# Optimization experiments

Hardware: AMD Instinct MI355X
Metric: run time of the kernel (lower is better)

The kernel has to match this reference:

```python
import jax, jax.numpy as jnp
import numpy as np

B, L, P, TPP, D, G = 4, 2, 100, 64, 768, 10  # batch, layers, passages, tokens/passage, hidden, n_tables
T = P * TPP


def setup_inputs() -> dict:
    key = jax.random.key(0)
    ks = jax.random.split(key, 12)
    s = 0.02  # weight init scale
    return {
        "answer_states": jax.random.normal(ks[0], (B, L, 1, D), jnp.float32),
        "query_passage_states": jax.random.normal(ks[1], (B, L, T, D), jnp.float32),
        "passage_masks": (jax.random.uniform(ks[2], (B, P, TPP)) < 0.9).astype(jnp.float32),
        "table_ids": jax.random.randint(ks[3], (B, P), 0, G, dtype=jnp.int32),
        "fusion_scores": jax.random.normal(ks[4], (B, P), jnp.float32),
        # learned params: passage_fnt (3D->D), table_fnt (3D->D), feat_l1 (2D->D), feat_l2 (D->1)
        "W_p": jax.random.normal(ks[5], (3 * D, D), jnp.float32) * s,
        "b_p": jnp.zeros((D,), jnp.float32),
        "W_t": jax.random.normal(ks[6], (3 * D, D), jnp.float32) * s,
        "b_t": jnp.zeros((D,), jnp.float32),
        "W1": jax.random.normal(ks[7], (2 * D, D), jnp.float32) * s,
        "b1": jnp.zeros((D,), jnp.float32),
        "W2": jax.random.normal(ks[8], (D, 1), jnp.float32) * s,
        "b2": jnp.zeros((1,), jnp.float32),
    }


def reference(answer_states, query_passage_states, passage_masks, table_ids,
              fusion_scores, W_p, b_p, W_t, b_t, W1, b1, W2, b2):
    # Use only the last layer, as in forward (states[:, -1:, :, :]).
    a = answer_states[:, -1:, :, :]                 # [B,1,1,D]
    q = query_passage_states[:, -1:, :, :]          # [B,1,T,D]
    a = jnp.broadcast_to(a, q.shape)
    x = jnp.concatenate([a, q, a * q], axis=-1)     # [B,1,T,3D]

    ps = (x @ W_p + b_p).reshape(B, 1, P, TPP, D)   # passage states
    ts = (x @ W_t + b_t).reshape(B, 1, P, TPP, D)   # per-passage table states

    # Group-by table_id max-pool over the passage axis, then broadcast back.
    def aggr_one(ts_i, tid):                        # ts_i: [1,P,TPP,D], tid: [P]
        data = jnp.moveaxis(ts_i, 1, 0)             # [P,1,TPP,D]
        seg_max = jax.ops.segment_max(data, tid, num_segments=G)  # [G,1,TPP,D]
        return jnp.moveaxis(seg_max[tid], 0, 1)     # [1,P,TPP,D]

    aggr = jax.vmap(aggr_one)(ts, table_ids)        # [B,1,P,TPP,D]

    feat = jnp.concatenate([ps, aggr], axis=-1)     # [B,1,P,TPP,2D]
    # feature_fnt: Linear -> ReLU -> (dropout = identity in eval) -> Linear
    h = jax.nn.relu(feat @ W1 + b1)                 # [B,1,P,TPP,D]
    scores = (h @ W2 + b2)[..., 0]                  # [B,1,P,TPP]

    masked = scores * passage_masks[:, None, :, :]  # broadcast mask over layers
    # sum over layers and tokens -> per-passage adapt scores
    out = masked.sum(axis=(1, 3))                   # [B,P]
    return out
```

## Files before the change

kernel.cpp:

```cpp
#include <hip/hip_runtime.h>
#include <hip/hip_bf16.h>

#define B_ 4
#define L_ 2
#define P_ 100
#define TPP_ 64
#define D_ 768
#define G_ 10
#define T_ (P_ * TPP_)
#define NC_ (2 * D_)

typedef __attribute__((ext_vector_type(8))) short bf16x8;
typedef __attribute__((ext_vector_type(4))) float f32x4;

__device__ __forceinline__ unsigned short f2bf(float f) {
    __hip_bfloat16 h = __float2bfloat16(f);
    return *reinterpret_cast<unsigned short*>(&h);
}
__device__ __forceinline__ float bfu2f(unsigned short u) {
    return __uint_as_float(((unsigned int)u) << 16);
}

__device__ __forceinline__ void gload_lds16(const void* g, void* l) {
    __builtin_amdgcn_global_load_lds(
        (const __attribute__((address_space(1))) void*)g,
        (__attribute__((address_space(3))) void*)l, 16, 0, 0);
}

#define SBAR()   __builtin_amdgcn_s_barrier()
#define SCHEDB() __builtin_amdgcn_sched_barrier(0)
#define VMCNT8() asm volatile("s_waitcnt vmcnt(8)" ::: "memory")
#define VMCNT0() asm volatile("s_waitcnt vmcnt(0)" ::: "memory")

__device__ __forceinline__ void stage64(
    const __hip_bfloat16* __restrict__ Ag, const __hip_bfloat16* __restrict__ Bg,
    int k0, __hip_bfloat16 (*As)[64], __hip_bfloat16 (*Bs)[64],
    int w, int row_l, int soff)
{
#pragma unroll
    for (int j = 0; j < 4; ++j) {
        int r = w * 32 + j * 8 + row_l;
        gload_lds16(Ag + (size_t)r * D_ + k0 + soff, &As[w * 32 + j * 8][0]);
        gload_lds16(Bg + (size_t)r * D_ + k0 + soff, &Bs[w * 32 + j * 8][0]);
    }
}

__device__ __forceinline__ void mfma_step64(
    __hip_bfloat16 (*As)[64], __hip_bfloat16 (*Bs)[64],
    int rr, int h, int wm, int wn, f32x4 acc[4][4])
{
#pragma unroll
    for (int ks = 0; ks < 2; ++ks) {
        const int rsl = (((ks << 2) + h) ^ (rr & 7)) << 3;
        bf16x8 af[4], bfr[4];
#pragma unroll
        for (int mi = 0; mi < 4; ++mi)
            af[mi] = *reinterpret_cast<const bf16x8*>(
                &As[wm * 64 + mi * 16 + rr][rsl]);
#pragma unroll
        for (int ni = 0; ni < 4; ++ni)
            bfr[ni] = *reinterpret_cast<const bf16x8*>(
                &Bs[wn * 64 + ni * 16 + rr][rsl]);
#pragma unroll
        for (int mi = 0; mi < 4; ++mi)
#pragma unroll
            for (int ni = 0; ni < 4; ++ni)
                acc[mi][ni] = __builtin_amdgcn_mfma_f32_16x16x32_bf16(
                    af[mi], bfr[ni], acc[mi][ni], 0, 0, 0);
    }
}

#define MFMA_STEP_P(As, Bs)                                                   \
    __builtin_amdgcn_s_setprio(1);                                            \
    mfma_step64(As, Bs, rr, h, wm, wn, acc);                                  \
    __builtin_amdgcn_s_setprio(0);

#define MFMA_LOOP_PIPE(Ag, Bg)                                                \
    {                                                                         \
        const int rr = lane & 15, h = lane >> 4;                              \
        const int row_l = lane >> 3;                                          \
        const int soff = ((lane & 7) ^ row_l) << 3;                           \
        stage64((Ag), (Bg), 0, As0, Bs0, w, row_l, soff);                     \
        stage64((Ag), (Bg), 64, As1, Bs1, w, row_l, soff);                    \
        SCHEDB();                                                             \
        for (int t = 0; t < 10; t += 2) {                                     \
            VMCNT8(); SBAR(); SCHEDB();                                       \
            MFMA_STEP_P(As0, Bs0);                                            \
            SCHEDB(); SBAR(); SCHEDB();                                       \
            stage64((Ag), (Bg), (t + 2) * 64, As0, Bs0, w, row_l, soff);      \
            SCHEDB();                                                         \
            VMCNT8(); SBAR(); SCHEDB();                                       \
            MFMA_STEP_P(As1, Bs1);                                            \
            SCHEDB(); SBAR(); SCHEDB();                                       \
            stage64((Ag), (Bg), (t + 3) * 64, As1, Bs1, w, row_l, soff);      \
            SCHEDB();                                                         \
        }                                                                     \
        VMCNT8(); SBAR(); SCHEDB();                                           \
        MFMA_STEP_P(As0, Bs0);                                   \
        SCHEDB();                                                             \
        VMCNT0(); SBAR(); SCHEDB();                                           \
        MFMA_STEP_P(As1, Bs1);                                   \
        __syncthreads();                                                      \
    }

#define DECL_LDS_DB()                                                         \
    __shared__ __align__(16) __hip_bfloat16 As0[128][64];                     \
    __shared__ __align__(16) __hip_bfloat16 Bs0[128][64];                     \
    __shared__ __align__(16) __hip_bfloat16 As1[128][64];                     \
    __shared__ __align__(16) __hip_bfloat16 Bs1[128][64];

#define DECL_ACC()                                                            \
    f32x4 acc[4][4];                                                          \
    _Pragma("unroll") for (int i = 0; i < 4; ++i)                             \
        _Pragma("unroll") for (int j = 0; j < 4; ++j)                         \
            _Pragma("unroll") for (int e = 0; e < 4; ++e) acc[i][j][e] = 0.0f;

__global__ __launch_bounds__(256) void prep_all(
    const float* __restrict__ answer, const float* __restrict__ W_p,
    const float* __restrict__ b_p, const float* __restrict__ W_t,
    const float* __restrict__ b_t, const float* __restrict__ W1,
    const float* __restrict__ qps, const int* __restrict__ tids,
    const float* __restrict__ mask, const float* __restrict__ b2,
    __hip_bfloat16* __restrict__ Wpe_nat, __hip_bfloat16* __restrict__ Wbig,
    float* __restrict__ c_p, float* __restrict__ c_t,
    __hip_bfloat16* __restrict__ qb, __hip_bfloat16* __restrict__ W1at,
    __hip_bfloat16* __restrict__ W1bt, int* __restrict__ glist,
    int* __restrict__ goff, float* __restrict__ out)
{
    __shared__ float lds[64][65];
    __shared__ float a_s[64];
    __shared__ float red2[2][4][64];
    __shared__ int g_cnt[B_][G_];
    __shared__ int g_off[B_][G_ + 1];
    __shared__ int g_cur[B_][G_];

    const int bid = blockIdx.x;
    const int tid = threadIdx.x;

    if (bid < 1152) {
        const int n0 = (bid % 24) * 64;
        const int k0 = ((bid / 24) % 12) * 64;
        const int b  = bid / 288;
        if (tid < 64) a_s[tid] = answer[((size_t)b * L_ + (L_ - 1)) * D_ + k0 + tid];
        __syncthreads();
        if (n0 < D_) {
#pragma unroll
            for (int i = 0; i < 16; ++i) {
                int k = (tid >> 6) + i * 4;
                int n = tid & 63;
                float v = W_p[(size_t)(D_ + k0 + k) * D_ + n0 + n] +
                          a_s[k] * W_p[(size_t)(2 * D_ + k0 + k) * D_ + n0 + n];
                Wpe_nat[(size_t)b * D_ * D_ + (size_t)(k0 + k) * D_ + n0 + n] =
                    __float2bfloat16(v);
            }
        } else {
            const int nn0 = n0 - D_;
#pragma unroll
            for (int i = 0; i < 16; ++i) {
                int k = (tid >> 6) + i * 4;
                int n = tid & 63;
                lds[k][n] = W_t[(size_t)(D_ + k0 + k) * D_ + nn0 + n] +
                            a_s[k] * W_t[(size_t)(2 * D_ + k0 + k) * D_ + nn0 + n];
            }
            __syncthreads();
#pragma unroll
            for (int j = 0; j < 16; ++j) {
                int n = (tid >> 6) + j * 4;
                int kk = tid & 63;
                Wbig[((size_t)b * NC_ + n0 + n) * D_ + k0 + kk] =
                    __float2bfloat16(lds[kk][n]);
            }
        }
    } else if (bid < 1200) {
        const int local = bid - 1152;
        const int b = local / 12;
        const int d = (local % 12) * 64 + (tid & 63);
        const int ks = tid >> 6;
        const float* a = answer + ((size_t)b * L_ + (L_ - 1)) * D_;
        float sp = 0.f, st = 0.f;
#pragma unroll 4
        for (int k = ks; k < D_; k += 4) {
            float av = a[k];
            sp += av * W_p[(size_t)k * D_ + d];
            st += av * W_t[(size_t)k * D_ + d];
        }
        red2[0][ks][tid & 63] = sp;
        red2[1][ks][tid & 63] = st;
        __syncthreads();
        if (ks == 0) {
            float s1 = b_p[d], s2 = b_t[d];
#pragma unroll
            for (int i = 0; i < 4; ++i) {
                s1 += red2[0][i][tid & 63];
                s2 += red2[1][i][tid & 63];
            }
            c_p[b * D_ + d] = s1;
            c_t[b * D_ + d] = s2;
        }
    } else if (bid < 1488) {
        const int local = bid - 1200;
        const int n0 = (local % 12) * 64;
        const int k0 = (local / 12) * 64;
#pragma unroll
        for (int i = 0; i < 16; ++i) {
            int k = (tid >> 6) + i * 4;
            int n = tid & 63;
            lds[k][n] = W1[(size_t)(k0 + k) * D_ + n0 + n];
        }
        __syncthreads();
        __hip_bfloat16* dst = (k0 < D_) ? W1at : W1bt;
        const int kk0 = (k0 < D_) ? k0 : k0 - D_;
#pragma unroll
        for (int j = 0; j < 16; ++j) {
            int n = (tid >> 6) + j * 4;
            int kk = tid & 63;
            dst[(size_t)(n0 + n) * D_ + kk0 + kk] = __float2bfloat16(lds[kk][n]);
        }
    } else if (bid == 1488) {
        if (tid < B_ * G_) g_cnt[tid / G_][tid % G_] = 0;
        __syncthreads();
        for (int i = tid; i < B_ * P_; i += 256)
            atomicAdd(&g_cnt[i / P_][tids[i]], 1);
        __syncthreads();
        if (tid < B_) {
            int o = 0;
            for (int g = 0; g < G_; ++g) { g_off[tid][g] = o; o += g_cnt[tid][g]; }
            g_off[tid][G_] = o;
            for (int g = 0; g <= G_; ++g) goff[tid * (G_ + 1) + g] = g_off[tid][g];
        }
        __syncthreads();
        if (tid < B_ * G_) g_cur[tid / G_][tid % G_] = g_off[tid / G_][tid % G_];
        __syncthreads();
        for (int i = tid; i < B_ * P_; i += 256) {
            int b = i / P_, p = i % P_;
            int slot = atomicAdd(&g_cur[b][tids[i]], 1);
            glist[b * P_ + slot] = p;
        }
    } else if (bid < 1491) {
        int bp = (bid - 1489) * 256 + tid;
        if (bp < B_ * P_) {
            float s = 0.f;
#pragma unroll 8
            for (int t = 0; t < TPP_; ++t) s += mask[(size_t)bp * TPP_ + t];
            out[bp] = s * b2[0];
        }
    } else {
        size_t base = ((size_t)(bid - 1491) * 256 + tid) * 8;
        int b = (int)(base / ((size_t)T_ * D_));
        size_t off = base % ((size_t)T_ * D_);
        const float4* src = reinterpret_cast<const float4*>(
            qps + ((size_t)b * L_ + (L_ - 1)) * (size_t)T_ * D_ + off);
        float4 v0 = src[0], v1 = src[1];
        bf16x8 o;
        o[0] = (short)f2bf(v0.x); o[1] = (short)f2bf(v0.y);
        o[2] = (short)f2bf(v0.z); o[3] = (short)f2bf(v0.w);
        o[4] = (short)f2bf(v1.x); o[5] = (short)f2bf(v1.y);
        o[6] = (short)f2bf(v1.z); o[7] = (short)f2bf(v1.w);
        *reinterpret_cast<bf16x8*>(&qb[base]) = o;
    }
}

__global__ __launch_bounds__(256) void fused_ts_c1(
    const __hip_bfloat16* __restrict__ qb, __hip_bfloat16* __restrict__ Wbig,
    const float* __restrict__ c_t, __hip_bfloat16* __restrict__ ts,
    const __hip_bfloat16* __restrict__ W1at,
    const __hip_bfloat16* __restrict__ Wpe_nat,
    const float* __restrict__ c_p, const float* __restrict__ W1,
    const float* __restrict__ b1, float* __restrict__ cc)
{
    DECL_LDS_DB();
    __shared__ float red[4][64];
    const int bid = blockIdx.x;
    const int tid = threadIdx.x;
    const int lane = tid & 63, w = tid >> 6;
    const int wm = w & 1, wn = w >> 1;

    if (bid < 1200) {
        const int swz = (bid & 7) * 150 + (bid >> 3);
        const int tn = swz % 6;
        const int tmb = swz / 6;
        const int tm = tmb % 50, b = tmb / 50;
        DECL_ACC();
        const __hip_bfloat16* Ag = qb + (size_t)b * T_ * D_ + (size_t)tm * 128 * D_;
        const __hip_bfloat16* Bg =
            Wbig + (size_t)b * NC_ * D_ + (size_t)(D_ + tn * 128) * D_;
        MFMA_LOOP_PIPE(Ag, Bg);
#pragma unroll
        for (int mi = 0; mi < 4; ++mi)
#pragma unroll
            for (int ni = 0; ni < 4; ++ni) {
                int col = tn * 128 + wn * 64 + ni * 16 + (lane & 15);
                int rb  = tm * 128 + wm * 64 + mi * 16 + (lane >> 4) * 4;
                float cv = c_t[b * D_ + col];
#pragma unroll
                for (int e = 0; e < 4; ++e)
                    ts[((size_t)b * T_ + rb + e) * D_ + col] =
                        __float2bfloat16(acc[mi][ni][e] + cv);
            }
    } else if (bid < 1344) {
        const int local = bid - 1200;
        const int tm = local % 6, tn = (local / 6) % 6, b = local / 36;
        DECL_ACC();
        const __hip_bfloat16* Ag = W1at + (size_t)tm * 128 * D_;
        const __hip_bfloat16* Bg =
            Wpe_nat + (size_t)b * D_ * D_ + (size_t)tn * 128 * D_;
        MFMA_LOOP_PIPE(Ag, Bg);
#pragma unroll
        for (int mi = 0; mi < 4; ++mi)
#pragma unroll
            for (int ni = 0; ni < 4; ++ni) {
                int col = tn * 128 + wn * 64 + ni * 16 + (lane & 15);
                int row = tm * 128 + wm * 64 + mi * 16 + (lane >> 4) * 4;
#pragma unroll
                for (int e = 0; e < 4; ++e)
                    Wbig[(size_t)b * NC_ * D_ + (size_t)(row + e) * D_ + col] =
                        __float2bfloat16(acc[mi][ni][e]);
            }
    } else {
        const int local = bid - 1344;
        const int b = local / 12;
        const int n = (local % 12) * 64 + (tid & 63);
        const int ks = tid >> 6;
        float s = 0.f;
#pragma unroll 4
        for (int d = ks; d < D_; d += 4)
            s += c_p[b * D_ + d] * W1[(size_t)d * D_ + n];
        red[ks][tid & 63] = s;
        __syncthreads();
        if (ks == 0) {
            float tot = b1[n];
#pragma unroll
            for (int i = 0; i < 4; ++i) tot += red[i][tid & 63];
            cc[b * D_ + n] = tot;
        }
    }
}

__global__ __launch_bounds__(256) void segmax_kernel(
    const __hip_bfloat16* __restrict__ ts, const int* __restrict__ glist,
    const int* __restrict__ goff, __hip_bfloat16* __restrict__ sm)
{
    int idx = blockIdx.x * 256 + threadIdx.x;
    int d4 = idx % (D_ / 4);
    int bt = idx / (D_ / 4);
    int t = bt % TPP_;
    int b = bt / TPP_;

    const ushort4* base =
        reinterpret_cast<const ushort4*>(ts + ((size_t)b * T_ + t) * D_) + d4;

    for (int g = 0; g < G_; ++g) {
        float m0 = -1e30f, m1 = -1e30f, m2 = -1e30f, m3 = -1e30f;
        int i0 = goff[b * (G_ + 1) + g], i1 = goff[b * (G_ + 1) + g + 1];
        for (int i = i0; i < i1; ++i) {
            int p = glist[b * P_ + i];
            ushort4 u = base[(size_t)p * TPP_ * (D_ / 4)];
            m0 = fmaxf(m0, bfu2f(u.x));
            m1 = fmaxf(m1, bfu2f(u.y));
            m2 = fmaxf(m2, bfu2f(u.z));
            m3 = fmaxf(m3, bfu2f(u.w));
        }
        ushort4 o;
        o.x = f2bf(m0); o.y = f2bf(m1); o.z = f2bf(m2); o.w = f2bf(m3);
        reinterpret_cast<ushort4*>(
            sm + (((size_t)b * G_ + g) * TPP_ + t) * D_)[d4] = o;
    }
}

__global__ __launch_bounds__(256) void gemm_smw(
    const __hip_bfloat16* __restrict__ sm, const __hip_bfloat16* __restrict__ W1bt,
    __hip_bfloat16* __restrict__ smW)
{
    const int swz = (blockIdx.x & 7) * 15 + (blockIdx.x >> 3);
    const int tn = swz % 6, tm = swz / 6;
    DECL_LDS_DB();
    const int tid = threadIdx.x;
    const int lane = tid & 63, w = tid >> 6;
    const int wm = w & 1, wn = w >> 1;
    DECL_ACC();

    const __hip_bfloat16* Ag = sm + (size_t)tm * 128 * D_;
    const __hip_bfloat16* Bg = W1bt + (size_t)tn * 128 * D_;
    MFMA_LOOP_PIPE(Ag, Bg);

#pragma unroll
    for (int mi = 0; mi < 4; ++mi)
#pragma unroll
        for (int ni = 0; ni < 4; ++ni) {
            int col = tn * 128 + wn * 64 + ni * 16 + (lane & 15);
            int rb  = tm * 128 + wm * 64 + mi * 16 + (lane >> 4) * 4;
#pragma unroll
            for (int e = 0; e < 4; ++e)
                smW[(size_t)(rb + e) * D_ + col] = __float2bfloat16(acc[mi][ni][e]);
        }
}

__global__ __launch_bounds__(256) void gemm_fin(
    const __hip_bfloat16* __restrict__ qb, const __hip_bfloat16* __restrict__ Wbig,
    const float* __restrict__ cc, const __hip_bfloat16* __restrict__ smW,
    const int* __restrict__ tids, const float* __restrict__ W2,
    const float* __restrict__ mask, float* __restrict__ out)
{
    const int swz = (blockIdx.x & 7) * 150 + (blockIdx.x >> 3);
    const int tn = swz % 6;
    const int tmb = swz / 6;
    const int tm = tmb % 50, b = tmb / 50;
    DECL_LDS_DB();
    __shared__ float rowsum[2][128];

    const int tid = threadIdx.x;
    const int lane = tid & 63, w = tid >> 6;
    const int wm = w & 1, wn = w >> 1;
    DECL_ACC();

    const __hip_bfloat16* Ag = qb + (size_t)b * T_ * D_ + (size_t)tm * 128 * D_;
    const __hip_bfloat16* Bg = Wbig + (size_t)b * NC_ * D_ + (size_t)tn * 128 * D_;
    MFMA_LOOP_PIPE(Ag, Bg);

    const int p = tm * 2 + wm;
    const int g = tids[b * P_ + p];
    const __hip_bfloat16* smWg = smW + ((size_t)(b * G_ + g) * TPP_) * D_;
    const int h = lane >> 4;

    float rs[4][4];
#pragma unroll
    for (int mi = 0; mi < 4; ++mi)
#pragma unroll
        for (int e = 0; e < 4; ++e) rs[mi][e] = 0.f;

#pragma unroll
    for (int ni = 0; ni < 4; ++ni) {
        int col = tn * 128 + wn * 64 + ni * 16 + (lane & 15);
        float ccv = cc[b * D_ + col];
        float w2v = W2[col];
#pragma unroll
        for (int mi = 0; mi < 4; ++mi)
#pragma unroll
            for (int e = 0; e < 4; ++e) {
                int trow = mi * 16 + h * 4 + e;
                float v = acc[mi][ni][e] + ccv +
                          bfu2f(*reinterpret_cast<const unsigned short*>(
                              &smWg[(size_t)trow * D_ + col]));
                rs[mi][e] += fmaxf(v, 0.f) * w2v;
            }
    }
#pragma unroll
    for (int off = 8; off >= 1; off >>= 1)
#pragma unroll
        for (int mi = 0; mi < 4; ++mi)
#pragma unroll
            for (int e = 0; e < 4; ++e) rs[mi][e] += __shfl_xor(rs[mi][e], off);

    if ((lane & 15) == 0) {
#pragma unroll
        for (int mi = 0; mi < 4; ++mi)
#pragma unroll
            for (int e = 0; e < 4; ++e)
                rowsum[wn][wm * 64 + mi * 16 + h * 4 + e] = rs[mi][e];
    }
    __syncthreads();

    if (tid < 128) {
        int pp = tid >> 6, t = tid & 63;
        float v = (rowsum[0][tid] + rowsum[1][tid]) *
                  mask[((size_t)b * P_ + tm * 2 + pp) * TPP_ + t];
#pragma unroll
        for (int off = 32; off >= 1; off >>= 1) v += __shfl_xor(v, off);
        if (t == 0) atomicAdd(&out[b * P_ + tm * 2 + pp], v);
    }
}

extern "C" void kernel_launch(void* const* d_in, const int* in_sizes, int n_in,
                              void* d_out, int out_size, void* d_ws, size_t ws_size,
                              hipStream_t stream)
{
    const float* answer = (const float*)d_in[0];
    const float* qps    = (const float*)d_in[1];
    const float* mask   = (const float*)d_in[2];
    const int*   tids   = (const int*)d_in[3];
    const float* W_p = (const float*)d_in[5];
    const float* b_p = (const float*)d_in[6];
    const float* W_t = (const float*)d_in[7];
    const float* b_t = (const float*)d_in[8];
    const float* W1  = (const float*)d_in[9];
    const float* b1  = (const float*)d_in[10];
    const float* W2  = (const float*)d_in[11];
    const float* b2  = (const float*)d_in[12];
    float* out = (float*)d_out;

    char* ws = (char*)d_ws;
    __hip_bfloat16* Wpe_nat = (__hip_bfloat16*)ws; ws += (size_t)B_ * D_ * D_ * 2;
    __hip_bfloat16* Wbig    = (__hip_bfloat16*)ws; ws += (size_t)B_ * NC_ * D_ * 2;
    float* c_p = (float*)ws;                   ws += (size_t)B_ * D_ * 4;
    float* c_t = (float*)ws;                   ws += (size_t)B_ * D_ * 4;
    float* cc  = (float*)ws;                   ws += (size_t)B_ * D_ * 4;
    __hip_bfloat16* qb = (__hip_bfloat16*)ws;  ws += (size_t)B_ * T_ * D_ * 2;
    __hip_bfloat16* ts = (__hip_bfloat16*)ws;  ws += (size_t)B_ * T_ * D_ * 2;
    __hip_bfloat16* sm = (__hip_bfloat16*)ws;  ws += (size_t)B_ * G_ * TPP_ * D_ * 2;
    __hip_bfloat16* smW = (__hip_bfloat16*)ws; ws += (size_t)B_ * G_ * TPP_ * D_ * 2;
    __hip_bfloat16* W1at = (__hip_bfloat16*)ws; ws += (size_t)D_ * D_ * 2;
    __hip_bfloat16* W1bt = (__hip_bfloat16*)ws; ws += (size_t)D_ * D_ * 2;
    int* glist = (int*)ws;                     ws += B_ * P_ * 4;
    int* goff  = (int*)ws;                     ws += B_ * (G_ + 1) * 4;

    prep_all<<<11091, 256, 0, stream>>>(
        answer, W_p, b_p, W_t, b_t, W1, qps, tids, mask, b2,
        Wpe_nat, Wbig, c_p, c_t, qb, W1at, W1bt, glist, goff, out);
    fused_ts_c1<<<1392, 256, 0, stream>>>(
        qb, Wbig, c_t, ts, W1at, Wpe_nat, c_p, W1, b1, cc);
    segmax_kernel<<<(B_ * TPP_ * (D_ / 4)) / 256, 256, 0, stream>>>(
        ts, glist, goff, sm);
    gemm_smw<<<120, 256, 0, stream>>>(sm, W1bt, smW);
    gemm_fin<<<1200, 256, 0, stream>>>(
        qb, Wbig, cc, smW, tids, W2, mask, out);
}
```

Baseline: 197.5 us.

## Switch GEMM main loop to triple-buffered 32-wide K stages

Replaces the double-buffered 64-wide K tile pipeline with a triple-buffered pipeline of 32-wide K tiles, changing the LDS swizzle and staging pattern to match. LDS use drops from 64 KB to 48 KB per block, which could allow higher occupancy, and the deeper prefetch gives more overlap of global loads with MFMA. The trade-off is twice as many barrier and waitcnt sync points per K, with less MFMA work between them.

```diff
diff --git a/kernel.cpp b/kernel.cpp
--- a/kernel.cpp
+++ b/kernel.cpp
@@ -30,84 +30,93 @@
 #define SBAR()   __builtin_amdgcn_s_barrier()
 #define SCHEDB() __builtin_amdgcn_sched_barrier(0)
 #define VMCNT8() asm volatile("s_waitcnt vmcnt(8)" ::: "memory")
+#define VMCNT4() asm volatile("s_waitcnt vmcnt(4)" ::: "memory")
 #define VMCNT0() asm volatile("s_waitcnt vmcnt(0)" ::: "memory")
 
-__device__ __forceinline__ void stage64(
+__device__ __forceinline__ void stage32(
     const __hip_bfloat16* __restrict__ Ag, const __hip_bfloat16* __restrict__ Bg,
-    int k0, __hip_bfloat16 (*As)[64], __hip_bfloat16 (*Bs)[64],
-    int w, int row_l, int soff)
-{
-#pragma unroll
-    for (int j = 0; j < 4; ++j) {
-        int r = w * 32 + j * 8 + row_l;
-        gload_lds16(Ag + (size_t)r * D_ + k0 + soff, &As[w * 32 + j * 8][0]);
-        gload_lds16(Bg + (size_t)r * D_ + k0 + soff, &Bs[w * 32 + j * 8][0]);
-    }
-}
-
-__device__ __forceinline__ void mfma_step64(
-    __hip_bfloat16 (*As)[64], __hip_bfloat16 (*Bs)[64],
-    int rr, int h, int wm, int wn, f32x4 acc[4][4])
-{
-#pragma unroll
-    for (int ks = 0; ks < 2; ++ks) {
-        const int rsl = (((ks << 2) + h) ^ (rr & 7)) << 3;
-        bf16x8 af[4], bfr[4];
-#pragma unroll
-        for (int mi = 0; mi < 4; ++mi)
-            af[mi] = *reinterpret_cast<const bf16x8*>(
-                &As[wm * 64 + mi * 16 + rr][rsl]);
+    int k0, __hip_bfloat16 (*As)[32], __hip_bfloat16 (*Bs)[32],
+    int w, int row16, int soff)
+{
+#pragma unroll
+    for (int j = 0; j < 2; ++j) {
+        int r = w * 32 + j * 16 + row16;
+        gload_lds16(Ag + (size_t)r * D_ + k0 + soff, &As[w * 32 + j * 16][0]);
+        gload_lds16(Bg + (size_t)r * D_ + k0 + soff, &Bs[w * 32 + j * 16][0]);
+    }
+}
+
+__device__ __forceinline__ void mfma_step32(
+    __hip_bfloat16 (*As)[32], __hip_bfloat16 (*Bs)[32],
+    int rr, int rsl, int wm, int wn, f32x4 acc[4][4])
+{
+    bf16x8 af[4], bfr[4];
+#pragma unroll
+    for (int mi = 0; mi < 4; ++mi)
+        af[mi] = *reinterpret_cast<const bf16x8*>(
+            &As[wm * 64 + mi * 16 + rr][rsl]);
+#pragma unroll
+    for (int ni = 0; ni < 4; ++ni)
+        bfr[ni] = *reinterpret_cast<const bf16x8*>(
+            &Bs[wn * 64 + ni * 16 + rr][rsl]);
+#pragma unroll
+    for (int mi = 0; mi < 4; ++mi)
 #pragma unroll
         for (int ni = 0; ni < 4; ++ni)
-            bfr[ni] = *reinterpret_cast<const bf16x8*>(
-                &Bs[wn * 64 + ni * 16 + rr][rsl]);
-#pragma unroll
-        for (int mi = 0; mi < 4; ++mi)
-#pragma unroll
-            for (int ni = 0; ni < 4; ++ni)
-                acc[mi][ni] = __builtin_amdgcn_mfma_f32_16x16x32_bf16(
-                    af[mi], bfr[ni], acc[mi][ni], 0, 0, 0);
-    }
+            acc[mi][ni] = __builtin_amdgcn_mfma_f32_16x16x32_bf16(
+                af[mi], bfr[ni], acc[mi][ni], 0, 0, 0);
 }
 
 #define MFMA_STEP_P(As, Bs)                                                   \
     __builtin_amdgcn_s_setprio(1);                                            \
-    mfma_step64(As, Bs, rr, h, wm, wn, acc);                                  \
+    mfma_step32(As, Bs, rr, rsl, wm, wn, acc);                                \
     __builtin_amdgcn_s_setprio(0);
 
 #define MFMA_LOOP_PIPE(Ag, Bg)                                                \
     {                                                                         \
         const int rr = lane & 15, h = lane >> 4;                              \
-        const int row_l = lane >> 3;                                          \
-        const int soff = ((lane & 7) ^ row_l) << 3;                           \
-        stage64((Ag), (Bg), 0, As0, Bs0, w, row_l, soff);                     \
-        stage64((Ag), (Bg), 64, As1, Bs1, w, row_l, soff);                    \
+        const int row16 = lane >> 2;                                          \
+        const int soff = ((lane & 3) ^ ((lane >> 3) & 3)) << 3;               \
+        const int rsl = (h ^ ((rr >> 1) & 3)) << 3;                           \
+        stage32((Ag), (Bg), 0,  As0, Bs0, w, row16, soff);                    \
+        stage32((Ag), (Bg), 32, As1, Bs1, w, row16, soff);                    \
+        stage32((Ag), (Bg), 64, As2, Bs2, w, row16, soff);                    \
         SCHEDB();                                                             \
-        for (int t = 0; t < 10; t += 2) {                                     \
+        for (int t = 0; t < 21; t += 3) {                                     \
             VMCNT8(); SBAR(); SCHEDB();                                       \
             MFMA_STEP_P(As0, Bs0);                                            \
             SCHEDB(); SBAR(); SCHEDB();                                       \
-            stage64((Ag), (Bg), (t + 2) * 64, As0, Bs0, w, row_l, soff);      \
+            stage32((Ag), (Bg), (t + 3) * 32, As0, Bs0, w, row16, soff);      \
             SCHEDB();                                                         \
             VMCNT8(); SBAR(); SCHEDB();                                       \
             MFMA_STEP_P(As1, Bs1);                                            \
             SCHEDB(); SBAR(); SCHEDB();                                       \
-            stage64((Ag), (Bg), (t + 3) * 64, As1, Bs1, w, row_l, soff);      \
+            stage32((Ag), (Bg), (t + 4) * 32, As1, Bs1, w, row16, soff);      \
+            SCHEDB();                                                         \
+            VMCNT8(); SBAR(); SCHEDB();                                       \
+            MFMA_STEP_P(As2, Bs2);                                            \
+            SCHEDB(); SBAR(); SCHEDB();                                       \
+            stage32((Ag), (Bg), (t + 5) * 32, As2, Bs2, w, row16, soff);      \
             SCHEDB();                                                         \
         }                                                                     \
         VMCNT8(); SBAR(); SCHEDB();                                           \
         MFMA_STEP_P(As0, Bs0);                                   \
         SCHEDB();                                                             \
+        VMCNT4(); SBAR(); SCHEDB();                                           \
+        MFMA_STEP_P(As1, Bs1);                                   \
+        SCHEDB();                                                             \
         VMCNT0(); SBAR(); SCHEDB();                                           \
-        MFMA_STEP_P(As1, Bs1);                                   \
+        MFMA_STEP_P(As2, Bs2);                                   \
         __syncthreads();                                                      \
     }
 
 #define DECL_LDS_DB()                                                         \
-    __shared__ __align__(16) __hip_bfloat16 As0[128][64];                     \
-    __shared__ __align__(16) __hip_bfloat16 Bs0[128][64];                     \
-    __shared__ __align__(16) __hip_bfloat16 As1[128][64];                     \
-    __shared__ __align__(16) __hip_bfloat16 Bs1[128][64];
+    __shared__ __align__(16) __hip_bfloat16 As0[128][32];           \
+    __shared__ __align__(16) __hip_bfloat16 Bs0[128][32];                     \
+    __shared__ __align__(16) __hip_bfloat16 As1[128][32];                     \
+    __shared__ __align__(16) __hip_bfloat16 Bs1[128][32];                     \
+    __shared__ __align__(16) __hip_bfloat16 As2[128][32];                     \
+    __shared__ __align__(16) __hip_bfloat16 Bs2[128][32];
 
 #define DECL_ACC()                                                            \
     f32x4 acc[4][4];                                                          \
```

Result: slower. 202.5 us (+2.5%).

## Fuse segment-max into ts GEMM epilogue via order-preserving atomicMax

Applied to the files above, without the earlier changes.

The ts GEMM epilogue no longer writes the full per-token table states to memory. Each element is encoded as an order-preserving uint and atomicMax'd directly into a per-(batch, table) buffer that prep_all zero-initialises. A small conversion kernel then decodes that buffer to bf16. This removes the large ts write/read and the separate segmax and grouping passes, at the cost of many global atomics with possible contention when several passages share a table, plus a new fp32-sized workspace.

```diff
diff --git a/kernel.cpp b/kernel.cpp
--- a/kernel.cpp
+++ b/kernel.cpp
@@ -31,6 +31,15 @@
 #define SCHEDB() __builtin_amdgcn_sched_barrier(0)
 #define VMCNT8() asm volatile("s_waitcnt vmcnt(8)" ::: "memory")
 #define VMCNT0() asm volatile("s_waitcnt vmcnt(0)" ::: "memory")
+
+__device__ __forceinline__ unsigned int fenc(float v) {
+    unsigned int bits = __float_as_uint(v);
+    return bits ^ (unsigned int)(((int)bits >> 31) | 0x80000000);
+}
+__device__ __forceinline__ float fdec(unsigned int k) {
+    unsigned int bits = (k & 0x80000000u) ? (k ^ 0x80000000u) : ~k;
+    return __uint_as_float(bits);
+}
 
 __device__ __forceinline__ void stage64(
     const __hip_bfloat16* __restrict__ Ag, const __hip_bfloat16* __restrict__ Bg,
@@ -119,20 +128,17 @@
     const float* __restrict__ answer, const float* __restrict__ W_p,
     const float* __restrict__ b_p, const float* __restrict__ W_t,
     const float* __restrict__ b_t, const float* __restrict__ W1,
-    const float* __restrict__ qps, const int* __restrict__ tids,
-    const float* __restrict__ mask, const float* __restrict__ b2,
+    const float* __restrict__ qps, const float* __restrict__ mask,
+    const float* __restrict__ b2,
     __hip_bfloat16* __restrict__ Wpe_nat, __hip_bfloat16* __restrict__ Wbig,
     float* __restrict__ c_p, float* __restrict__ c_t,
     __hip_bfloat16* __restrict__ qb, __hip_bfloat16* __restrict__ W1at,
-    __hip_bfloat16* __restrict__ W1bt, int* __restrict__ glist,
-    int* __restrict__ goff, float* __restrict__ out)
+    __hip_bfloat16* __restrict__ W1bt, unsigned int* __restrict__ smU,
+    float* __restrict__ out)
 {
     __shared__ float lds[64][65];
     __shared__ float a_s[64];
     __shared__ float red2[2][4][64];
-    __shared__ int g_cnt[B_][G_];
-    __shared__ int g_off[B_][G_ + 1];
-    __shared__ int g_cur[B_][G_];
 
     const int bid = blockIdx.x;
     const int tid = threadIdx.x;
@@ -216,36 +222,16 @@
             int kk = tid & 63;
             dst[(size_t)(n0 + n) * D_ + kk0 + kk] = __float2bfloat16(lds[kk][n]);
         }
-    } else if (bid == 1488) {
-        if (tid < B_ * G_) g_cnt[tid / G_][tid % G_] = 0;
-        __syncthreads();
-        for (int i = tid; i < B_ * P_; i += 256)
-            atomicAdd(&g_cnt[i / P_][tids[i]], 1);
-        __syncthreads();
-        if (tid < B_) {
-            int o = 0;
-            for (int g = 0; g < G_; ++g) { g_off[tid][g] = o; o += g_cnt[tid][g]; }
-            g_off[tid][G_] = o;
-            for (int g = 0; g <= G_; ++g) goff[tid * (G_ + 1) + g] = g_off[tid][g];
-        }
-        __syncthreads();
-        if (tid < B_ * G_) g_cur[tid / G_][tid % G_] = g_off[tid / G_][tid % G_];
-        __syncthreads();
-        for (int i = tid; i < B_ * P_; i += 256) {
-            int b = i / P_, p = i % P_;
-            int slot = atomicAdd(&g_cur[b][tids[i]], 1);
-            glist[b * P_ + slot] = p;
-        }
-    } else if (bid < 1491) {
-        int bp = (bid - 1489) * 256 + tid;
+    } else if (bid < 1490) {
+        int bp = (bid - 1488) * 256 + tid;
         if (bp < B_ * P_) {
             float s = 0.f;
 #pragma unroll 8
             for (int t = 0; t < TPP_; ++t) s += mask[(size_t)bp * TPP_ + t];
             out[bp] = s * b2[0];
         }
-    } else {
-        size_t base = ((size_t)(bid - 1491) * 256 + tid) * 8;
+    } else if (bid < 11090) {
+        size_t base = ((size_t)(bid - 1490) * 256 + tid) * 8;
         int b = (int)(base / ((size_t)T_ * D_));
         size_t off = base % ((size_t)T_ * D_);
         const float4* src = reinterpret_cast<const float4*>(
@@ -257,12 +243,18 @@
         o[4] = (short)f2bf(v1.x); o[5] = (short)f2bf(v1.y);
         o[6] = (short)f2bf(v1.z); o[7] = (short)f2bf(v1.w);
         *reinterpret_cast<bf16x8*>(&qb[base]) = o;
+    } else {
+        size_t base = ((size_t)(bid - 11090) * 256 + tid) * 8;
+        uint4 z = {0u, 0u, 0u, 0u};
+        *reinterpret_cast<uint4*>(&smU[base]) = z;
+        *reinterpret_cast<uint4*>(&smU[base + 4]) = z;
     }
 }
 
 __global__ __launch_bounds__(256) void fused_ts_c1(
     const __hip_bfloat16* __restrict__ qb, __hip_bfloat16* __restrict__ Wbig,
-    const float* __restrict__ c_t, __hip_bfloat16* __restrict__ ts,
+    const float* __restrict__ c_t, const int* __restrict__ tids,
+    unsigned int* __restrict__ smU,
     const __hip_bfloat16* __restrict__ W1at,
     const __hip_bfloat16* __restrict__ Wpe_nat,
     const float* __restrict__ c_p, const float* __restrict__ W1,
@@ -285,18 +277,24 @@
         const __hip_bfloat16* Bg =
             Wbig + (size_t)b * NC_ * D_ + (size_t)(D_ + tn * 128) * D_;
         MFMA_LOOP_PIPE(Ag, Bg);
-#pragma unroll
-        for (int mi = 0; mi < 4; ++mi)
-#pragma unroll
-            for (int ni = 0; ni < 4; ++ni) {
-                int col = tn * 128 + wn * 64 + ni * 16 + (lane & 15);
-                int rb  = tm * 128 + wm * 64 + mi * 16 + (lane >> 4) * 4;
-                float cv = c_t[b * D_ + col];
-#pragma unroll
-                for (int e = 0; e < 4; ++e)
-                    ts[((size_t)b * T_ + rb + e) * D_ + col] =
-                        __float2bfloat16(acc[mi][ni][e] + cv);
-            }
+
+        const int p = tm * 2 + wm;
+        const int g = tids[b * P_ + p];
+        unsigned int* smb = smU + ((size_t)(b * G_ + g) * TPP_) * D_;
+        const int h = lane >> 4;
+#pragma unroll
+        for (int ni = 0; ni < 4; ++ni) {
+            int col = tn * 128 + wn * 64 + ni * 16 + (lane & 15);
+            float cv = c_t[b * D_ + col];
+#pragma unroll
+            for (int mi = 0; mi < 4; ++mi)
+#pragma unroll
+                for (int e = 0; e < 4; ++e) {
+                    int t = mi * 16 + h * 4 + e;
+                    atomicMax(&smb[(size_t)t * D_ + col],
+                              fenc(acc[mi][ni][e] + cv));
+                }
+        }
     } else if (bid < 1344) {
         const int local = bid - 1200;
         const int tm = local % 6, tn = (local / 6) % 6, b = local / 36;
@@ -336,35 +334,18 @@
     }
 }
 
-__global__ __launch_bounds__(256) void segmax_kernel(
-    const __hip_bfloat16* __restrict__ ts, const int* __restrict__ glist,
-    const int* __restrict__ goff, __hip_bfloat16* __restrict__ sm)
-{
-    int idx = blockIdx.x * 256 + threadIdx.x;
-    int d4 = idx % (D_ / 4);
-    int bt = idx / (D_ / 4);
-    int t = bt % TPP_;
-    int b = bt / TPP_;
-
-    const ushort4* base =
-        reinterpret_cast<const ushort4*>(ts + ((size_t)b * T_ + t) * D_) + d4;
-
-    for (int g = 0; g < G_; ++g) {
-        float m0 = -1e30f, m1 = -1e30f, m2 = -1e30f, m3 = -1e30f;
-        int i0 = goff[b * (G_ + 1) + g], i1 = goff[b * (G_ + 1) + g + 1];
-        for (int i = i0; i < i1; ++i) {
-            int p = glist[b * P_ + i];
-            ushort4 u = base[(size_t)p * TPP_ * (D_ / 4)];
-            m0 = fmaxf(m0, bfu2f(u.x));
-            m1 = fmaxf(m1, bfu2f(u.y));
-            m2 = fmaxf(m2, bfu2f(u.z));
-            m3 = fmaxf(m3, bfu2f(u.w));
-        }
-        ushort4 o;
-        o.x = f2bf(m0); o.y = f2bf(m1); o.z = f2bf(m2); o.w = f2bf(m3);
-        reinterpret_cast<ushort4*>(
-            sm + (((size_t)b * G_ + g) * TPP_ + t) * D_)[d4] = o;
-    }
+__global__ __launch_bounds__(256) void sm_convert(
+    const unsigned int* __restrict__ smU, __hip_bfloat16* __restrict__ sm)
+{
+    size_t base = ((size_t)blockIdx.x * 256 + threadIdx.x) * 8;
+    uint4 u0 = *reinterpret_cast<const uint4*>(&smU[base]);
+    uint4 u1 = *reinterpret_cast<const uint4*>(&smU[base + 4]);
+    bf16x8 o;
+    o[0] = (short)f2bf(fdec(u0.x)); o[1] = (short)f2bf(fdec(u0.y));
+    o[2] = (short)f2bf(fdec(u0.z)); o[3] = (short)f2bf(fdec(u0.w));
+    o[4] = (short)f2bf(fdec(u1.x)); o[5] = (short)f2bf(fdec(u1.y));
+    o[6] = (short)f2bf(fdec(u1.z)); o[7] = (short)f2bf(fdec(u1.w));
+    *reinterpret_cast<bf16x8*>(&sm[base]) = o;
 }
 
 __global__ __launch_bounds__(256) void gemm_smw(
@@ -495,21 +476,18 @@
     float* c_t = (float*)ws;                   ws += (size_t)B_ * D_ * 4;
     float* cc  = (float*)ws;                   ws += (size_t)B_ * D_ * 4;
     __hip_bfloat16* qb = (__hip_bfloat16*)ws;  ws += (size_t)B_ * T_ * D_ * 2;
-    __hip_bfloat16* ts = (__hip_bfloat16*)ws;  ws += (size_t)B_ * T_ * D_ * 2;
+    unsigned int* smU = (unsigned int*)ws;     ws += (size_t)B_ * G_ * TPP_ * D_ * 4;
     __hip_bfloat16* sm = (__hip_bfloat16*)ws;  ws += (size_t)B_ * G_ * TPP_ * D_ * 2;
     __hip_bfloat16* smW = (__hip_bfloat16*)ws; ws += (size_t)B_ * G_ * TPP_ * D_ * 2;
     __hip_bfloat16* W1at = (__hip_bfloat16*)ws; ws += (size_t)D_ * D_ * 2;
     __hip_bfloat16* W1bt = (__hip_bfloat16*)ws; ws += (size_t)D_ * D_ * 2;
-    int* glist = (int*)ws;                     ws += B_ * P_ * 4;
-    int* goff  = (int*)ws;                     ws += B_ * (G_ + 1) * 4;
-
-    prep_all<<<11091, 256, 0, stream>>>(
-        answer, W_p, b_p, W_t, b_t, W1, qps, tids, mask, b2,
-        Wpe_nat, Wbig, c_p, c_t, qb, W1at, W1bt, glist, goff, out);
+
+    prep_all<<<12050, 256, 0, stream>>>(
+        answer, W_p, b_p, W_t, b_t, W1, qps, mask, b2,
+        Wpe_nat, Wbig, c_p, c_t, qb, W1at, W1bt, smU, out);
     fused_ts_c1<<<1392, 256, 0, stream>>>(
-        qb, Wbig, c_t, ts, W1at, Wpe_nat, c_p, W1, b1, cc);
-    segmax_kernel<<<(B_ * TPP_ * (D_ / 4)) / 256, 256, 0, stream>>>(
-        ts, glist, goff, sm);
+        qb, Wbig, c_t, tids, smU, W1at, Wpe_nat, c_p, W1, b1, cc);
+    sm_convert<<<960, 256, 0, stream>>>(smU, sm);
     gemm_smw<<<120, 256, 0, stream>>>(sm, W1bt, smW);
     gemm_fin<<<1200, 256, 0, stream>>>(
         qb, Wbig, cc, smW, tids, W2, mask, out);
```

Result: faster. 174.8 us (-11.5%).
